# Performance work log

Measured on AMD Instinct MI355X. Metric: run time of the kernel, lower is better.

## Reference

```python
import jax, jax.numpy as jnp
import numpy as np

B, S, F = 8, 2048, 1024
NEG = -1000000000.0

def setup_inputs() -> dict:
    key = jax.random.key(0)
    ks = jax.random.split(key, 8)
    x = jax.random.normal(ks[0], (B, S, F), dtype=jnp.float32)
    # causal attention mask [S, S], 1 = keep, 0 = masked
    attn_mask = jnp.tril(jnp.ones((S, S), dtype=jnp.int32))
    # key padding mask [B, 1, S], random 0/1
    pad_mask = jax.random.randint(ks[1], (B, 1, S), 0, 2, dtype=jnp.int32)
    # ensure at least the first key position is valid per batch to avoid all-masked rows
    pad_mask = pad_mask.at[:, :, 0].set(1)
    sc = 1.0 / np.sqrt(F).astype(np.float32)
    Wq = jax.random.normal(ks[2], (F, F), dtype=jnp.float32) * sc
    bq = jax.random.normal(ks[3], (F,), dtype=jnp.float32) * 0.01
    Wk = jax.random.normal(ks[4], (F, F), dtype=jnp.float32) * sc
    bk = jax.random.normal(ks[5], (F,), dtype=jnp.float32) * 0.01
    Wv = jax.random.normal(ks[6], (F, F), dtype=jnp.float32) * sc
    bv = jax.random.normal(ks[7], (F,), dtype=jnp.float32) * 0.01
    return {"x": x, "attn_mask": attn_mask, "pad_mask": pad_mask,
            "Wq": Wq, "bq": bq, "Wk": Wk, "bk": bk, "Wv": Wv, "bv": bv}

def reference(x, attn_mask, pad_mask, Wq, bq, Wk, bk, Wv, bv):
    # torch Linear: y = x @ W.T + b
    q = jnp.einsum('bsf,of->bso', x, Wq) + bq
    k = jnp.einsum('bsf,of->bso', x, Wk) + bk
    v = jnp.einsum('bsf,of->bso', x, Wv) + bv
    scale = 1.0 / jnp.sqrt(jnp.asarray(q.shape[-1], dtype=x.dtype))
    scores = jnp.einsum('bqf,bkf->bqk', q, k) * scale  # [B, S, S]
    scores = jnp.where(pad_mask == 0, NEG, scores)            # pad_mask [B,1,S] broadcasts
    scores = jnp.where(attn_mask[None, :, :] == 0, NEG, scores)
    prob = jax.nn.softmax(scores, axis=-1)
    # dropout=0.0 (eval / identity)
    return jnp.einsum('bqk,bkf->bqf', prob, v)
```

## Files before the change

kernel.cpp:

```cpp
#include <hip/hip_runtime.h>
#include <hip/hip_bf16.h>
#include <stdint.h>


#define S_LEN 2048
#define F_DIM 1024
#define NBATCH 8
#define BS_TOT (NBATCH * S_LEN)

typedef __attribute__((ext_vector_type(8))) short bf16x8;
typedef __attribute__((ext_vector_type(4))) float f32x4;
typedef unsigned short u16;

__device__ __forceinline__ u16 f32_to_bf16_rne(float f) {
    union { float f; uint32_t u; } v; v.f = f;
    uint32_t u = v.u;
    u += 0x7FFFu + ((u >> 16) & 1u);
    return (u16)(u >> 16);
}
__device__ __forceinline__ float bf16_to_f32(u16 h) {
    union { uint32_t u; float f; } v; v.u = ((uint32_t)h) << 16;
    return v.f;
}

__device__ __forceinline__ void gload_lds16(const u16* g, u16* l) {
    __builtin_amdgcn_global_load_lds(
        (const __attribute__((address_space(1))) void*)g,
        (__attribute__((address_space(3))) void*)l,
        16, 0, 0);
}

__global__ __launch_bounds__(256) void cvt_f32_bf16(const float* __restrict__ in,
                                                    u16* __restrict__ out, int n) {
    int i = (blockIdx.x * 256 + threadIdx.x) * 4;
    if (i + 3 < n) {
        float4 f = *(const float4*)(in + i);
        ushort4 o;
        o.x = f32_to_bf16_rne(f.x); o.y = f32_to_bf16_rne(f.y);
        o.z = f32_to_bf16_rne(f.z); o.w = f32_to_bf16_rne(f.w);
        *(ushort4*)(out + i) = o;
    }
}

__global__ __launch_bounds__(256) void cvt_w3(const float* __restrict__ Wq,
                                              const float* __restrict__ Wk,
                                              const float* __restrict__ Wv,
                                              u16* __restrict__ Wb) {
    const int which = blockIdx.y;
    const float* in = (which == 0) ? Wq : (which == 1) ? Wk : Wv;
    int i = (blockIdx.x * 256 + threadIdx.x) * 4;
    float4 f = *(const float4*)(in + i);
    ushort4 o;
    o.x = f32_to_bf16_rne(f.x); o.y = f32_to_bf16_rne(f.y);
    o.z = f32_to_bf16_rne(f.z); o.w = f32_to_bf16_rne(f.w);
    *(ushort4*)(Wb + (size_t)which * F_DIM * F_DIM + i) = o;
}

__global__ __launch_bounds__(256) void k_scan(const int* __restrict__ pad,
                                              int* __restrict__ sIdx,
                                              int* __restrict__ kneed) {
    const int b = blockIdx.x;
    const int tid = threadIdx.x;
    const int* p = pad + b * S_LEN;
    __shared__ int part[256];
    __shared__ int cnt_s;
    int v[8]; int sum = 0; const int s0 = tid * 8;
#pragma unroll
    for (int i = 0; i < 8; i++) { v[i] = p[s0 + i]; sum += v[i]; }
    part[tid] = sum;
    __syncthreads();
    if (tid == 0) {
        int acc = 0;
        for (int i = 0; i < 256; i++) { int t = part[i]; part[i] = acc; acc += t; }
        cnt_s = acc;
    }
    __syncthreads();
    int run = part[tid];
#pragma unroll
    for (int i = 0; i < 8; i++) {
        const int s = s0 + i;
        if (v[i]) sIdx[b * S_LEN + run] = s;
        run += v[i];
    }
    const int cnt = cnt_s;
    for (int c = cnt + tid; c < S_LEN; c += 256) sIdx[b * S_LEN + c] = S_LEN;
    if (tid < 16) {
        const int et = (tid + 1) * 16 - 1;
        kneed[b * 16 + tid] = (et == 255) ? cnt : part[et + 1];
    }
}

__global__ __launch_bounds__(256) void k_gather(const u16* __restrict__ xb,
                                                const int* __restrict__ sIdx,
                                                const int* __restrict__ kneed,
                                                u16* __restrict__ xc) {
    const int b = blockIdx.x >> 11, c = blockIdx.x & 2047;
    if (c >= kneed[b * 16 + 15]) return;
    const int s = sIdx[b * S_LEN + c];
    const ushort4 v = *(const ushort4*)(xb + ((size_t)b * S_LEN + s) * F_DIM
                                        + threadIdx.x * 4);
    *(ushort4*)(xc + ((size_t)b * S_LEN + c) * F_DIM + threadIdx.x * 4) = v;
}

template<class Epi>
__device__ __forceinline__ void gemm_tile_128(
    const u16* __restrict__ A, int lda,
    const u16* __restrict__ Bt, int ldb,
    int m0, int n0, int K, float alpha, Epi epi)
{
    __shared__ u16 la[128 * 32];
    __shared__ u16 lb[128 * 32];

    const int tid  = threadIdx.x;
    const int lane = tid & 63;
    const int wave = tid >> 6;
    const int wm = (wave & 1) * 64;
    const int wn = (wave >> 1) * 64;

    f32x4 acc[4][4];
#pragma unroll
    for (int mt = 0; mt < 4; mt++)
#pragma unroll
        for (int nt = 0; nt < 4; nt++)
            acc[mt][nt] = f32x4{0.f, 0.f, 0.f, 0.f};

    const int mrow = wm + (lane & 15);
    const int nrow = wn + (lane & 15);
    const int koff = (lane >> 4) * 8;

    const int cb0 = wave * 64;
    const int cb1 = wave * 64 + 256;
    const int lrow = lane >> 2;
    const int lcol = (lane & 3) * 8;
    const u16* pa0 = A  + (size_t)(m0 + (cb0 >> 2) + lrow) * lda + lcol;
    const u16* pa1 = A  + (size_t)(m0 + (cb1 >> 2) + lrow) * lda + lcol;
    const u16* pb0 = Bt + (size_t)(n0 + (cb0 >> 2) + lrow) * ldb + lcol;
    const u16* pb1 = Bt + (size_t)(n0 + (cb1 >> 2) + lrow) * ldb + lcol;
    u16* qa0 = la + cb0 * 8;
    u16* qa1 = la + cb1 * 8;
    u16* qb0 = lb + cb0 * 8;
    u16* qb1 = lb + cb1 * 8;

    for (int kk = 0; kk < K; kk += 32) {
        __syncthreads();
        gload_lds16(pa0 + kk, qa0);
        gload_lds16(pa1 + kk, qa1);
        gload_lds16(pb0 + kk, qb0);
        gload_lds16(pb1 + kk, qb1);
        __syncthreads();

        bf16x8 fa[4], fb[4];
#pragma unroll
        for (int t = 0; t < 4; t++) {
            fa[t] = *(const bf16x8*)(la + (mrow + t * 16) * 32 + koff);
            fb[t] = *(const bf16x8*)(lb + (nrow + t * 16) * 32 + koff);
        }
#pragma unroll
        for (int mt = 0; mt < 4; mt++)
#pragma unroll
            for (int nt = 0; nt < 4; nt++)
                acc[mt][nt] = __builtin_amdgcn_mfma_f32_16x16x32_bf16(
                    fa[mt], fb[nt], acc[mt][nt], 0, 0, 0);
    }

    const int col   = lane & 15;
    const int rquad = (lane >> 4) * 4;
#pragma unroll
    for (int mt = 0; mt < 4; mt++)
#pragma unroll
        for (int nt = 0; nt < 4; nt++) {
            const int n = n0 + wn + nt * 16 + col;
#pragma unroll
            for (int r = 0; r < 4; r++) {
                const int m = m0 + wm + mt * 16 + rquad + r;
                epi(m, n, acc[mt][nt][r] * alpha);
            }
        }
}

__global__ __launch_bounds__(256) void k_qkv(const u16* __restrict__ xb,
                                             const u16* __restrict__ xc,
                                             const u16* __restrict__ Wb,
                                             const float* __restrict__ bq,
                                             const float* __restrict__ bk,
                                             const float* __restrict__ bv,
                                             const int* __restrict__ kneed,
                                             u16* __restrict__ q,
                                             u16* __restrict__ kc,
                                             u16* __restrict__ vTc) {
    const int which = blockIdx.y;
    const int bx = blockIdx.x;
    const int xcd = bx & 7;
    const int idx = bx >> 3;
    const int m0 = (xcd * 16 + (idx >> 3)) * 128;
    const int n0 = (idx & 7) * 128;
    const int b  = m0 >> 11;
    const int cnt = kneed[b * 16 + 15];
    if (which > 0 && (m0 & 2047) >= cnt) return;
    const float* bias = (which == 0) ? bq : (which == 1) ? bk : bv;
    const u16* W = Wb + (size_t)which * F_DIM * F_DIM;
    const u16* A = (which == 0) ? xb : xc;
    if (which < 2) {
        u16* o = (which == 0) ? q : kc;
        gemm_tile_128(A, F_DIM, W, F_DIM, m0, n0, F_DIM, 1.0f,
            [&](int m, int n, float v) {
                o[(size_t)m * F_DIM + n] = f32_to_bf16_rne(v + bias[n]);
            });
    } else {
        gemm_tile_128(A, F_DIM, W, F_DIM, m0, n0, F_DIM, 1.0f,
            [&](int m, int n, float v) {
                const int c = m & 2047;
                vTc[((size_t)b * F_DIM + n) * S_LEN + c] =
                    (c < cnt) ? f32_to_bf16_rne(v + bias[n]) : (u16)0;
            });
    }
}

__global__ __launch_bounds__(256) void k_scores(const u16* __restrict__ q,
                                                const u16* __restrict__ kc,
                                                const int* __restrict__ sIdx,
                                                const int* __restrict__ kneed,
                                                u16* __restrict__ Pp,
                                                float* __restrict__ lsum) {
    const int b = blockIdx.x & 7;
    const int t = blockIdx.x >> 3;
    int it = 0, base = 0;
    while (base + it + 1 <= t) { base += it + 1; it++; }
    const int jt = t - base;
    if (jt * 128 >= kneed[b * 16 + it]) return;
    const int* sIb = sIdx + b * S_LEN;
    u16* Pb = Pp + (size_t)b * S_LEN * S_LEN;

    float rs[16];
#pragma unroll
    for (int i = 0; i < 16; i++) rs[i] = 0.f;

    gemm_tile_128(q + (size_t)b * S_LEN * F_DIM, F_DIM,
                  kc + (size_t)b * S_LEN * F_DIM, F_DIM,
                  it * 128, jt * 128, F_DIM, 0.03125f,
        [&](int m, int n, float v) {
            u16 o = 0;
            if (sIb[n] <= m)
                o = f32_to_bf16_rne(__expf(v - 16.0f));
            Pb[(size_t)m * S_LEN + n] = o;
            const int i = m & 63;
            rs[((i >> 4) << 2) | (i & 3)] += bf16_to_f32(o);
        });

    const int lane  = threadIdx.x & 63;
    const int wave  = threadIdx.x >> 6;
    const int wm    = (wave & 1) * 64;
    const int rquad = (lane >> 4) * 4;
    float* lb = lsum + b * S_LEN + it * 128 + wm;
#pragma unroll
    for (int i = 0; i < 16; i++) {
        float s = rs[i];
        s += __shfl_xor(s, 1);
        s += __shfl_xor(s, 2);
        s += __shfl_xor(s, 4);
        s += __shfl_xor(s, 8);
        if ((lane & 15) == 0)
            atomicAdd(&lb[((i >> 2) << 4) + rquad + (i & 3)], s);
    }
}

__global__ __launch_bounds__(256) void k_pv(const u16* __restrict__ Pp,
                                            const u16* __restrict__ vTc,
                                            const float* __restrict__ lsum,
                                            const int* __restrict__ kneed,
                                            float* __restrict__ out) {
    const int b = blockIdx.x & 7;
    const int rest = blockIdx.x >> 3;
    const int j = rest >> 3;
    const int nt = rest & 7;
    const int it = (j & 1) ? (j >> 1) : (15 - (j >> 1));
    const int Keff = (kneed[b * 16 + it] + 127) & ~127;
    const float* ls = lsum + b * S_LEN;
    float* ob = out + (size_t)b * S_LEN * F_DIM;

    const int lane  = threadIdx.x & 63;
    const int wave  = threadIdx.x >> 6;
    const int wm    = (wave & 1) * 64;
    const int rquad = (lane >> 4) * 4;
    const int mb    = it * 128 + wm;
    float myinv[16];
#pragma unroll
    for (int i = 0; i < 16; i++)
        myinv[i] = 1.0f / ls[mb + ((i >> 2) << 4) + rquad + (i & 3)];

    gemm_tile_128(Pp + (size_t)b * S_LEN * S_LEN, S_LEN,
                  vTc + (size_t)b * F_DIM * S_LEN, S_LEN,
                  it * 128, nt * 128, Keff, 1.0f,
        [&](int m, int n, float v) {
            const int i = m & 63;
            ob[(size_t)m * F_DIM + n] = v * myinv[((i >> 4) << 2) | (i & 3)];
        });
}

extern "C" void kernel_launch(void* const* d_in, const int* in_sizes, int n_in,
                              void* d_out, int out_size, void* d_ws, size_t ws_size,
                              hipStream_t stream) {
    const float* x  = (const float*)d_in[0];
    const int* pad  = (const int*)d_in[2];
    const float* Wq = (const float*)d_in[3];
    const float* bq = (const float*)d_in[4];
    const float* Wk = (const float*)d_in[5];
    const float* bk = (const float*)d_in[6];
    const float* Wv = (const float*)d_in[7];
    const float* bv = (const float*)d_in[8];
    float* out = (float*)d_out;

    char* ws = (char*)d_ws;
    u16* q    = (u16*)(ws);
    u16* kc   = (u16*)(ws + 32ull * 1024 * 1024);
    u16* vTc  = (u16*)(ws + 64ull * 1024 * 1024);
    u16* Pp   = (u16*)(ws + 96ull * 1024 * 1024);
    u16* xc   = (u16*)(ws + 96ull * 1024 * 1024);
    u16* xb   = (u16*)(ws + 160ull * 1024 * 1024);
    u16* Wb   = (u16*)(ws + 192ull * 1024 * 1024);
    float* il = (float*)(ws + 200ull * 1024 * 1024);
    int* sIdx = (int*)(ws + 202ull * 1024 * 1024);
    int* kneed= (int*)(ws + 203ull * 1024 * 1024);

    const int BSF = BS_TOT * F_DIM;
    const int FF = F_DIM * F_DIM;

    hipMemsetAsync(il, 0, BS_TOT * sizeof(float), stream);

    cvt_f32_bf16<<<BSF / 1024, 256, 0, stream>>>(x, xb, BSF);
    cvt_w3<<<dim3(FF / 1024, 3), 256, 0, stream>>>(Wq, Wk, Wv, Wb);
    k_scan<<<NBATCH, 256, 0, stream>>>(pad, sIdx, kneed);
    k_gather<<<BS_TOT, 256, 0, stream>>>(xb, sIdx, kneed, xc);

    k_qkv<<<dim3(1024, 3), 256, 0, stream>>>(xb, xc, Wb, bq, bk, bv, kneed,
                                             q, kc, vTc);

    k_scores<<<1088, 256, 0, stream>>>(q, kc, sIdx, kneed, Pp, il);

    k_pv<<<1024, 256, 0, stream>>>(Pp, vTc, il, kneed, out);
}
```

Measured before the change: 335.3 us.

## Split QKV projection into Q and KV kernels with 256-row tiles for KV

Replaces the fused QKV kernel with a separate Q kernel and a K/V kernel. The K/V kernel uses 512 threads and 256x128 tiles, indexed per batch so blocks past the valid key count exit early. Larger M tiles reuse each B-tile load across more rows, and the per-batch indexing skips more padded rows at finer granularity. The cost is two launches instead of one, more LDS per block, and possibly lower occupancy.

```diff
diff --git a/kernel.cpp b/kernel.cpp
--- a/kernel.cpp
+++ b/kernel.cpp
@@ -178,42 +178,116 @@
         }
 }
 
-__global__ __launch_bounds__(256) void k_qkv(const u16* __restrict__ xb,
-                                             const u16* __restrict__ xc,
-                                             const u16* __restrict__ Wb,
-                                             const float* __restrict__ bq,
-                                             const float* __restrict__ bk,
-                                             const float* __restrict__ bv,
-                                             const int* __restrict__ kneed,
-                                             u16* __restrict__ q,
-                                             u16* __restrict__ kc,
-                                             u16* __restrict__ vTc) {
-    const int which = blockIdx.y;
+template<class Epi>
+__device__ __forceinline__ void gemm_tile_256m(
+    const u16* __restrict__ A, int lda,
+    const u16* __restrict__ Bt, int ldb,
+    int m0, int n0, int K, float alpha, Epi epi)
+{
+    __shared__ u16 la[256 * 32];
+    __shared__ u16 lb[128 * 32];
+
+    const int tid  = threadIdx.x;
+    const int lane = tid & 63;
+    const int wave = tid >> 6;
+    const int wm = (wave & 3) * 64;
+    const int wn = (wave >> 2) * 64;
+
+    f32x4 acc[4][4];
+#pragma unroll
+    for (int mt = 0; mt < 4; mt++)
+#pragma unroll
+        for (int nt = 0; nt < 4; nt++)
+            acc[mt][nt] = f32x4{0.f, 0.f, 0.f, 0.f};
+
+    const int mrow = wm + (lane & 15);
+    const int nrow = wn + (lane & 15);
+    const int koff = (lane >> 4) * 8;
+
+    const int wvo  = wave * 512;
+    const int lrow = wave * 16 + (lane >> 2);
+    const int lcol = (lane & 3) * 8;
+    const u16* pa0 = A  + (size_t)(m0 + lrow) * lda + lcol;
+    const u16* pa1 = A  + (size_t)(m0 + 128 + lrow) * lda + lcol;
+    const u16* pb0 = Bt + (size_t)(n0 + lrow) * ldb + lcol;
+
+    for (int kk = 0; kk < K; kk += 32) {
+        __syncthreads();
+        gload_lds16(pa0 + kk, la + wvo);
+        gload_lds16(pa1 + kk, la + 4096 + wvo);
+        gload_lds16(pb0 + kk, lb + wvo);
+        __syncthreads();
+
+        bf16x8 fa[4], fb[4];
+#pragma unroll
+        for (int t = 0; t < 4; t++) {
+            fa[t] = *(const bf16x8*)(la + (mrow + t * 16) * 32 + koff);
+            fb[t] = *(const bf16x8*)(lb + (nrow + t * 16) * 32 + koff);
+        }
+#pragma unroll
+        for (int mt = 0; mt < 4; mt++)
+#pragma unroll
+            for (int nt = 0; nt < 4; nt++)
+                acc[mt][nt] = __builtin_amdgcn_mfma_f32_16x16x32_bf16(
+                    fa[mt], fb[nt], acc[mt][nt], 0, 0, 0);
+    }
+
+    const int col   = lane & 15;
+    const int rquad = (lane >> 4) * 4;
+#pragma unroll
+    for (int mt = 0; mt < 4; mt++)
+#pragma unroll
+        for (int nt = 0; nt < 4; nt++) {
+            const int n = n0 + wn + nt * 16 + col;
+#pragma unroll
+            for (int r = 0; r < 4; r++) {
+                const int m = m0 + wm + mt * 16 + rquad + r;
+                epi(m, n, acc[mt][nt][r] * alpha);
+            }
+        }
+}
+
+__global__ __launch_bounds__(256) void k_q(const u16* __restrict__ xb,
+                                           const u16* __restrict__ Wb,
+                                           const float* __restrict__ bq,
+                                           u16* __restrict__ q) {
     const int bx = blockIdx.x;
     const int xcd = bx & 7;
     const int idx = bx >> 3;
     const int m0 = (xcd * 16 + (idx >> 3)) * 128;
     const int n0 = (idx & 7) * 128;
-    const int b  = m0 >> 11;
+    gemm_tile_128(xb, F_DIM, Wb, F_DIM, m0, n0, F_DIM, 1.0f,
+        [&](int m, int n, float v) {
+            q[(size_t)m * F_DIM + n] = f32_to_bf16_rne(v + bq[n]);
+        });
+}
+
+__global__ __launch_bounds__(512) void k_kv(const u16* __restrict__ xc,
+                                            const u16* __restrict__ Wb,
+                                            const float* __restrict__ bk,
+                                            const float* __restrict__ bv,
+                                            const int* __restrict__ kneed,
+                                            u16* __restrict__ kc,
+                                            u16* __restrict__ vTc) {
+    const int which = blockIdx.y;
+    const int bx = blockIdx.x;
+    const int b = bx & 7;
+    const int t = bx >> 3;
+    const int m0 = (t >> 3) * 256;
+    const int n0 = (t & 7) * 128;
     const int cnt = kneed[b * 16 + 15];
-    if (which > 0 && (m0 & 2047) >= cnt) return;
-    const float* bias = (which == 0) ? bq : (which == 1) ? bk : bv;
-    const u16* W = Wb + (size_t)which * F_DIM * F_DIM;
-    const u16* A = (which == 0) ? xb : xc;
-    if (which < 2) {
-        u16* o = (which == 0) ? q : kc;
-        gemm_tile_128(A, F_DIM, W, F_DIM, m0, n0, F_DIM, 1.0f,
-            [&](int m, int n, float v) {
-                o[(size_t)m * F_DIM + n] = f32_to_bf16_rne(v + bias[n]);
-            });
-    } else {
-        gemm_tile_128(A, F_DIM, W, F_DIM, m0, n0, F_DIM, 1.0f,
-            [&](int m, int n, float v) {
-                const int c = m & 2047;
-                vTc[((size_t)b * F_DIM + n) * S_LEN + c] =
-                    (c < cnt) ? f32_to_bf16_rne(v + bias[n]) : (u16)0;
-            });
-    }
+    if (m0 >= cnt) return;
+    const float* bias = which ? bv : bk;
+    const u16* W = Wb + (size_t)(which + 1) * F_DIM * F_DIM;
+    const u16* A = xc + (size_t)b * S_LEN * F_DIM;
+    gemm_tile_256m(A, F_DIM, W, F_DIM, m0, n0, F_DIM, 1.0f,
+        [&](int m, int n, float v) {
+            const u16 h = f32_to_bf16_rne(v + bias[n]);
+            if (which == 0)
+                kc[((size_t)b * S_LEN + m) * F_DIM + n] = h;
+            else
+                vTc[((size_t)b * F_DIM + n) * S_LEN + m] = (m < cnt) ? h : (u16)0;
+        });
 }
 
 __global__ __launch_bounds__(256) void k_scores(const u16* __restrict__ q,
@@ -332,8 +406,8 @@
     k_scan<<<NBATCH, 256, 0, stream>>>(pad, sIdx, kneed);
     k_gather<<<BS_TOT, 256, 0, stream>>>(xb, sIdx, kneed, xc);
 
-    k_qkv<<<dim3(1024, 3), 256, 0, stream>>>(xb, xc, Wb, bq, bk, bv, kneed,
-                                             q, kc, vTc);
+    k_q<<<1024, 256, 0, stream>>>(xb, Wb, bq, q);
+    k_kv<<<dim3(512, 2), 512, 0, stream>>>(xc, Wb, bk, bv, kneed, kc, vTc);
 
     k_scores<<<1088, 256, 0, stream>>>(q, kc, sIdx, kneed, Pp, il);
 
```

New measurement: 375.2 us. 1.12x slower.
